# Optimization experiments

Measured on AMD Instinct MI355X. Metric: run time of the kernel, lower is better.

Reference implementation:

```python
import jax, jax.numpy as jnp
import numpy as np

N = 8192          # number of candidate boxes
NUM_CLASSES = 80  # COCO-style class count
IOU_THRESHOLD = 0.45


def setup_inputs() -> dict:
    key = jax.random.key(0)
    k1, k2, k3, k4 = jax.random.split(key, 4)
    # valid xyxy boxes: top-left in [0,1000), width/height in [1,101)
    xy = jax.random.uniform(k1, (N, 2)) * 1000.0
    wh = jax.random.uniform(k2, (N, 2)) * 100.0 + 1.0
    boxes = jnp.concatenate([xy, xy + wh], axis=1)            # [N,4]
    scores = jax.random.uniform(k3, (N,))                     # [N], all > 0
    idxs = jax.random.randint(k4, (N,), 0, NUM_CLASSES)       # [N] class ids
    return {"boxes": boxes, "scores": scores, "idxs": idxs}


def _nms_keep_mask(boxes, scores, iou_thr):
    """Greedy NMS (torchvision semantics) on a single set of boxes.
    Returns a boolean keep mask in the ORIGINAL box order."""
    n = boxes.shape[0]
    order = jnp.argsort(-scores)          # score-descending priority
    b = boxes[order]                      # [n,4]
    area = (b[:, 2] - b[:, 0]) * (b[:, 3] - b[:, 1])
    lt = jnp.maximum(b[:, None, :2], b[None, :, :2])   # [n,n,2]
    rb = jnp.minimum(b[:, None, 2:], b[None, :, 2:])   # [n,n,2]
    wh = jnp.clip(rb - lt, 0.0)
    inter = wh[..., 0] * wh[..., 1]                    # [n,n]
    iou = inter / (area[:, None] + area[None, :] - inter)
    over = iou > iou_thr                               # [n,n] bool
    lower_priority = jnp.arange(n)

    def body(i, suppressed):
        kept_i = jnp.logical_not(suppressed[i])
        # a kept box suppresses all lower-priority boxes it overlaps too much
        return suppressed | (kept_i & over[i] & (lower_priority > i))

    suppressed = jax.lax.fori_loop(0, n, body, jnp.zeros((n,), bool))
    # scatter keep decisions back to original order
    return jnp.zeros((n,), bool).at[order].set(~suppressed)


def reference(boxes, scores, idxs):
    iou_threshold = IOU_THRESHOLD
    # per-class coordinate offsets make boxes of different classes disjoint,
    # so one global NMS == the per-class NMS loop of the torch module
    max_coordinate = boxes.max()
    offsets = idxs.astype(boxes.dtype) * (max_coordinate + 1.0)
    boxes_for_nms = boxes + offsets[:, None]
    keep_mask = _nms_keep_mask(boxes_for_nms, scores, iou_threshold)
    # suppressed boxes get score 0 (all real scores are > 0), so after the
    # descending sort the kept boxes occupy the leading rows exactly as in
    # the torch module; suppressed boxes pad the tail (fixed output shape).
    scores_after_nms = jnp.where(keep_mask, scores, 0.0)
    inds = jnp.argsort(-scores_after_nms)      # [N] keep indices, score-desc
    sorted_scores = scores_after_nms[inds]
    out_boxes = jnp.concatenate([boxes[inds], sorted_scores[:, None]], axis=-1)
    return (out_boxes, inds)
```

## Files before the change

kernel.cpp:

```cpp
#include <hip/hip_runtime.h>
#include <stdint.h>

#define NBOX 8192
#define NW   128
#define IOU_THR 0.45f
#define NCLS 80
#define NSEG NCLS
#define SEGCAP 128
#define CLSCAP 256
#define ENT_LDS 2560
#define TAIL_BLOCKS 8

typedef unsigned long long u64;
typedef unsigned int u32;
typedef unsigned short u16;

__global__ void __launch_bounds__(256) k_pm(const float4* __restrict__ boxes4,
                                            const int* __restrict__ idxs,
                                            const float* __restrict__ scores,
                                            ulonglong2* __restrict__ ent,
                                            u32* __restrict__ entCnt,
                                            u16* __restrict__ rank16g) {
    int b = blockIdx.x, t = threadIdx.x;
    if (b < NCLS) {
        __shared__ float4 lb[CLSCAP];
        __shared__ float  la[CLSCAP];
        __shared__ int    lj[CLSCAP];
        __shared__ float  red[256];
        __shared__ u32    ccnt, lcnt;
        float mx = 0.0f;
        for (int i = t; i < NBOX; i += 256) {
            float4 v = boxes4[i];
            mx = fmaxf(mx, fmaxf(fmaxf(v.x, v.y), fmaxf(v.z, v.w)));
        }
        red[t] = mx;
        __syncthreads();
        for (int s = 128; s > 0; s >>= 1) {
            if (t < s) red[t] = fmaxf(red[t], red[t + s]);
            __syncthreads();
        }
        float mc1 = red[0] + 1.0f;
        float off = (float)b * mc1;
        if (t == 0) { ccnt = 0; lcnt = 0; }
        __syncthreads();
        for (int j = t; j < NBOX; j += 256) {
            if (idxs[j] == b) {
                u32 x = atomicAdd(&ccnt, 1u);
                if (x < CLSCAP) {
                    float4 bx = boxes4[j];
                    bx.x += off; bx.y += off; bx.z += off; bx.w += off;
                    lb[x] = bx;
                    la[x] = (bx.z - bx.x) * (bx.w - bx.y);
                    lj[x] = j;
                }
            }
        }
        __syncthreads();
        u32 cnt = min(ccnt, (u32)CLSCAP);
        if ((u32)t < cnt) {
            float4 bv = lb[t];
            float  av = la[t];
            int    jv = lj[t];
            for (u32 u = 0; u < (u32)t; ++u) {
                float4 bu = lb[u];
                float ltx = fmaxf(bu.x, bv.x), lty = fmaxf(bu.y, bv.y);
                float rbx = fminf(bu.z, bv.z), rby = fminf(bu.w, bv.w);
                float wx = fmaxf(rbx - ltx, 0.0f), wy = fmaxf(rby - lty, 0.0f);
                float inter = wx * wy;
                if (inter > 0.0f) {
                    float iou = inter / (la[u] + av - inter);
                    if (iou > IOU_THR) {
                        u32 x = atomicAdd(&lcnt, 1u);
                        if (x < SEGCAP) {
                            int iu = lj[u];
                            ulonglong2 e;
                            e.x = 1ULL << (iu & 63);
                            e.y = (u64)(((u32)jv << 7) | ((u32)iu >> 6));
                            ent[b * SEGCAP + x] = e;
                        }
                    }
                }
            }
        }
        __syncthreads();
        if (t == 0) entCnt[b] = min(lcnt, (u32)SEGCAP);
    } else {
        __shared__ u64 lk[2048];
        __shared__ u16 part[256];
        int rb = b - NCLS;
        int jj = rb * 32 + (t & 31);
        u64 kj = ((u64)(~__float_as_uint(scores[jj])) << 32) | (u32)jj;
        int cnt = 0;
        int p = t >> 5;
        for (int ch = 0; ch < 4; ++ch) {
            for (int i = t; i < 2048; i += 256) {
                int g = ch * 2048 + i;
                lk[i] = ((u64)(~__float_as_uint(scores[g])) << 32) | (u32)g;
            }
            __syncthreads();
            int base = p * 256;
#pragma unroll 8
            for (int i = 0; i < 256; ++i) cnt += (lk[base + i] < kj) ? 1 : 0;
            __syncthreads();
        }
        part[t] = (u16)cnt;
        __syncthreads();
        if (t < 32) {
            int s = 0;
#pragma unroll
            for (int q = 0; q < 8; ++q) s += part[q * 32 + t];
            rank16g[rb * 32 + t] = (u16)s;
        }
    }
}

__global__ void __launch_bounds__(1024)
k_tail(const ulonglong2* __restrict__ ent, const u32* __restrict__ entCnt,
       const u16* __restrict__ rank16g, const float4* __restrict__ boxes4,
       const float* __restrict__ scores, ulonglong2* __restrict__ gEnt,
       u64* __restrict__ gLT, float* __restrict__ out) {
    __shared__ ulonglong2 sE[ENT_LDS];
    __shared__ u64 sLT[ENT_LDS];
    __shared__ u16 rank16[NBOX];
    __shared__ u32 scnt[NSEG], soff[NSEG];
    __shared__ u64 kw[NW], sup[NW], kws[NW];
    __shared__ u32 wps[NW], wpo[NW];
    __shared__ u32 s_nk;
    __shared__ int chg;

    int t = threadIdx.x;
    if (t < NSEG) scnt[t] = entCnt[t];
    for (int j = t; j < NBOX; j += 1024) rank16[j] = rank16g[j];
    if (t < NW) { kw[t] = ~0ULL; kws[t] = 0ULL; }
    __syncthreads();
    if (t < 64) {
        u32 c0 = (2 * t < NSEG) ? scnt[2 * t] : 0u;
        u32 c1 = (2 * t + 1 < NSEG) ? scnt[2 * t + 1] : 0u;
        u32 s = c0 + c1;
        for (int d = 1; d < 64; d <<= 1) { u32 v = __shfl_up(s, d, 64); if (t >= d) s += v; }
        u32 ex = s - c0 - c1;
        if (2 * t < NSEG) soff[2 * t] = ex;
        if (2 * t + 1 < NSEG) soff[2 * t + 1] = ex + c0;
    }
    __syncthreads();
    u32 n = soff[NSEG - 1] + scnt[NSEG - 1];
    bool fits = (n <= (u32)ENT_LDS);
    for (u32 idx = t; idx < NSEG * SEGCAP; idx += 1024) {
        u32 seg = idx >> 7, l = idx & 127u;
        if (l < scnt[seg]) {
            ulonglong2 E = ent[idx];
            u32 d = soff[seg] + l;
            if (fits) sE[d] = E; else gEnt[d] = E;
        }
    }
    __syncthreads();
    for (u32 e = t; e < n; e += 1024) {
        ulonglong2 E = fits ? sE[e] : gEnt[e];
        u32 meta = (u32)E.y;
        u32 ej = meta >> 7, ew = meta & 127u;
        u32 rj = rank16[ej];
        u64 lt = 0, wrem = E.x;
        while (wrem) {
            int bb = __ffsll(wrem) - 1;
            wrem &= wrem - 1;
            if (rank16[ew * 64 + bb] < rj) lt |= (1ULL << bb);
        }
        if (fits) sLT[e] = lt; else gLT[e] = lt;
    }
    __syncthreads();

    for (int iter = 0; iter < NBOX; ++iter) {
        if (t < NW) sup[t] = 0ULL;
        if (t == 0) chg = 0;
        __syncthreads();
        for (u32 e = t; e < n; e += 1024) {
            ulonglong2 E = fits ? sE[e] : gEnt[e];
            u64 lt      = fits ? sLT[e] : gLT[e];
            u32 meta = (u32)E.y;
            u32 ej = meta >> 7, ew = meta & 127u;
            u64 word = E.x;
            if (word & lt & kw[ew])
                atomicOr(&sup[ej >> 6], 1ULL << (ej & 63u));
            u64 rev = word & ~lt;
            if (rev && ((kw[ej >> 6] >> (ej & 63u)) & 1ULL))
                atomicOr(&sup[ew], rev);
        }
        __syncthreads();
        if (t < NW) {
            u64 nk2 = ~sup[t];
            if (nk2 != kw[t]) { kw[t] = nk2; chg = 1; }
        }
        __syncthreads();
        int dn = !chg;
        __syncthreads();
        if (dn) break;
    }

    for (int j = t; j < NBOX; j += 1024) {
        if ((kw[j >> 6] >> (j & 63)) & 1ULL) {
            u32 r = rank16[j];
            atomicOr(&kws[r >> 6], 1ULL << (r & 63u));
        }
    }
    __syncthreads();
    if (t < 64) {
        int l = t;
        u32 a0 = (u32)__popcll(kws[2 * l]), a1 = (u32)__popcll(kws[2 * l + 1]);
        u32 s = a0 + a1;
        for (int d = 1; d < 64; d <<= 1) { u32 v = __shfl_up(s, d, 64); if (l >= d) s += v; }
        u32 ex = s - a0 - a1;
        wps[2 * l] = ex; wps[2 * l + 1] = ex + a0;
        if (l == 63) s_nk = s;
        u32 b0 = (u32)__popcll(kw[2 * l]), b1 = (u32)__popcll(kw[2 * l + 1]);
        u32 so = b0 + b1;
        for (int d = 1; d < 64; d <<= 1) { u32 v = __shfl_up(so, d, 64); if (l >= d) so += v; }
        u32 exo = so - b0 - b1;
        wpo[2 * l] = exo; wpo[2 * l + 1] = exo + b0;
    }
    __syncthreads();
    u32 nk = s_nk;

    int j = blockIdx.x * 1024 + t;
    if (j < NBOX) {
        bool kept = (kw[j >> 6] >> (j & 63)) & 1ULL;
        u32 pos;
        if (kept) {
            u32 r = rank16[j];
            pos = wps[r >> 6] + (u32)__popcll(kws[r >> 6] & ((1ULL << (r & 63)) - 1ULL));
        } else {
            u32 prefO = wpo[j >> 6] + (u32)__popcll(kw[j >> 6] & ((1ULL << (j & 63)) - 1ULL));
            pos = nk + (u32)j - prefO;
        }
        float4 bx = boxes4[j];
        float s = kept ? scores[j] : 0.0f;
        out[pos * 5 + 0] = bx.x;
        out[pos * 5 + 1] = bx.y;
        out[pos * 5 + 2] = bx.z;
        out[pos * 5 + 3] = bx.w;
        out[pos * 5 + 4] = s;
        out[NBOX * 5 + pos] = (float)j;
    }
}

extern "C" void kernel_launch(void* const* d_in, const int* in_sizes, int n_in,
                              void* d_out, int out_size, void* d_ws, size_t ws_size,
                              hipStream_t stream) {
    const float* boxes  = (const float*)d_in[0];
    const float* scores = (const float*)d_in[1];
    const int*   idxs   = (const int*)d_in[2];
    float* out = (float*)d_out;

    char* w = (char*)d_ws;
    ulonglong2* ent    = (ulonglong2*)(w + 0);
    ulonglong2* gEnt   = (ulonglong2*)(w + 163840);
    u64*        gLT    = (u64*)       (w + 327680);
    u16*        rank16 = (u16*)       (w + 409600);
    u32*        entCnt = (u32*)       (w + 425984);

    k_pm<<<NCLS + 256, 256, 0, stream>>>((const float4*)boxes, idxs, scores, ent, entCnt, rank16);
    k_tail<<<TAIL_BLOCKS, 1024, 0, stream>>>(ent, entCnt, rank16, (const float4*)boxes,
                                             scores, gEnt, gLT, out);
}
```

Baseline: 44.48 us.

## Encode overlap edges as directed winner-loser pairs in a packed u32

Result: slower. 45.73 us (median of 2 runs) (+2.8%).

```diff
diff --git a/kernel.cpp b/kernel.cpp
--- a/kernel.cpp
+++ b/kernel.cpp
@@ -5,10 +5,9 @@
 #define NW   128
 #define IOU_THR 0.45f
 #define NCLS 80
-#define NSEG NCLS
 #define SEGCAP 128
 #define CLSCAP 256
-#define ENT_LDS 2560
+#define EDGE_LDS 2048
 #define TAIL_BLOCKS 8
 
 typedef unsigned long long u64;
@@ -18,13 +17,14 @@
 __global__ void __launch_bounds__(256) k_pm(const float4* __restrict__ boxes4,
                                             const int* __restrict__ idxs,
                                             const float* __restrict__ scores,
-                                            ulonglong2* __restrict__ ent,
+                                            u32* __restrict__ ent,
                                             u32* __restrict__ entCnt,
                                             u16* __restrict__ rank16g) {
     int b = blockIdx.x, t = threadIdx.x;
     if (b < NCLS) {
         __shared__ float4 lb[CLSCAP];
         __shared__ float  la[CLSCAP];
+        __shared__ float  ls[CLSCAP];
         __shared__ int    lj[CLSCAP];
         __shared__ float  red[256];
         __shared__ u32    ccnt, lcnt;
@@ -51,6 +51,7 @@
                     bx.x += off; bx.y += off; bx.z += off; bx.w += off;
                     lb[x] = bx;
                     la[x] = (bx.z - bx.x) * (bx.w - bx.y);
+                    ls[x] = scores[j];
                     lj[x] = j;
                 }
             }
@@ -60,6 +61,7 @@
         if ((u32)t < cnt) {
             float4 bv = lb[t];
             float  av = la[t];
+            float  sv = ls[t];
             int    jv = lj[t];
             for (u32 u = 0; u < (u32)t; ++u) {
                 float4 bu = lb[u];
@@ -70,14 +72,13 @@
                 if (inter > 0.0f) {
                     float iou = inter / (la[u] + av - inter);
                     if (iou > IOU_THR) {
+                        float su = ls[u];
+                        int   iu = lj[u];
+                        bool uwin = (su > sv) || (su == sv && iu < jv);
+                        u32 winI  = uwin ? (u32)iu : (u32)jv;
+                        u32 loseI = uwin ? (u32)jv : (u32)iu;
                         u32 x = atomicAdd(&lcnt, 1u);
-                        if (x < SEGCAP) {
-                            int iu = lj[u];
-                            ulonglong2 e;
-                            e.x = 1ULL << (iu & 63);
-                            e.y = (u64)(((u32)jv << 7) | ((u32)iu >> 6));
-                            ent[b * SEGCAP + x] = e;
-                        }
+                        if (x < SEGCAP) ent[b * SEGCAP + x] = (loseI << 13) | winI;
                     }
                 }
             }
@@ -115,75 +116,42 @@
 }
 
 __global__ void __launch_bounds__(1024)
-k_tail(const ulonglong2* __restrict__ ent, const u32* __restrict__ entCnt,
+k_tail(const u32* __restrict__ ent, const u32* __restrict__ entCnt,
        const u16* __restrict__ rank16g, const float4* __restrict__ boxes4,
-       const float* __restrict__ scores, ulonglong2* __restrict__ gEnt,
-       u64* __restrict__ gLT, float* __restrict__ out) {
-    __shared__ ulonglong2 sE[ENT_LDS];
-    __shared__ u64 sLT[ENT_LDS];
+       const float* __restrict__ scores, float* __restrict__ out) {
+    __shared__ u32 sedge[EDGE_LDS];
     __shared__ u16 rank16[NBOX];
-    __shared__ u32 scnt[NSEG], soff[NSEG];
+    __shared__ u32 scnt[NCLS];
     __shared__ u64 kw[NW], sup[NW], kws[NW];
     __shared__ u32 wps[NW], wpo[NW];
-    __shared__ u32 s_nk;
+    __shared__ u32 s_m, s_nk;
     __shared__ int chg;
 
     int t = threadIdx.x;
-    if (t < NSEG) scnt[t] = entCnt[t];
+    if (t < NCLS) scnt[t] = entCnt[t];
     for (int j = t; j < NBOX; j += 1024) rank16[j] = rank16g[j];
     if (t < NW) { kw[t] = ~0ULL; kws[t] = 0ULL; }
-    __syncthreads();
-    if (t < 64) {
-        u32 c0 = (2 * t < NSEG) ? scnt[2 * t] : 0u;
-        u32 c1 = (2 * t + 1 < NSEG) ? scnt[2 * t + 1] : 0u;
-        u32 s = c0 + c1;
-        for (int d = 1; d < 64; d <<= 1) { u32 v = __shfl_up(s, d, 64); if (t >= d) s += v; }
-        u32 ex = s - c0 - c1;
-        if (2 * t < NSEG) soff[2 * t] = ex;
-        if (2 * t + 1 < NSEG) soff[2 * t + 1] = ex + c0;
-    }
-    __syncthreads();
-    u32 n = soff[NSEG - 1] + scnt[NSEG - 1];
-    bool fits = (n <= (u32)ENT_LDS);
-    for (u32 idx = t; idx < NSEG * SEGCAP; idx += 1024) {
+    if (t == 0) s_m = 0;
+    __syncthreads();
+    for (u32 idx = t; idx < NCLS * SEGCAP; idx += 1024) {
         u32 seg = idx >> 7, l = idx & 127u;
         if (l < scnt[seg]) {
-            ulonglong2 E = ent[idx];
-            u32 d = soff[seg] + l;
-            if (fits) sE[d] = E; else gEnt[d] = E;
-        }
-    }
-    __syncthreads();
-    for (u32 e = t; e < n; e += 1024) {
-        ulonglong2 E = fits ? sE[e] : gEnt[e];
-        u32 meta = (u32)E.y;
-        u32 ej = meta >> 7, ew = meta & 127u;
-        u32 rj = rank16[ej];
-        u64 lt = 0, wrem = E.x;
-        while (wrem) {
-            int bb = __ffsll(wrem) - 1;
-            wrem &= wrem - 1;
-            if (rank16[ew * 64 + bb] < rj) lt |= (1ULL << bb);
-        }
-        if (fits) sLT[e] = lt; else gLT[e] = lt;
-    }
-    __syncthreads();
+            u32 pos = atomicAdd(&s_m, 1u);
+            if (pos < (u32)EDGE_LDS) sedge[pos] = ent[idx];
+        }
+    }
+    __syncthreads();
+    u32 n = min(s_m, (u32)EDGE_LDS);
 
     for (int iter = 0; iter < NBOX; ++iter) {
         if (t < NW) sup[t] = 0ULL;
         if (t == 0) chg = 0;
         __syncthreads();
         for (u32 e = t; e < n; e += 1024) {
-            ulonglong2 E = fits ? sE[e] : gEnt[e];
-            u64 lt      = fits ? sLT[e] : gLT[e];
-            u32 meta = (u32)E.y;
-            u32 ej = meta >> 7, ew = meta & 127u;
-            u64 word = E.x;
-            if (word & lt & kw[ew])
-                atomicOr(&sup[ej >> 6], 1ULL << (ej & 63u));
-            u64 rev = word & ~lt;
-            if (rev && ((kw[ej >> 6] >> (ej & 63u)) & 1ULL))
-                atomicOr(&sup[ew], rev);
+            u32 ed = sedge[e];
+            u32 winI = ed & 8191u, loseI = ed >> 13;
+            if ((kw[winI >> 6] >> (winI & 63u)) & 1ULL)
+                atomicOr(&sup[loseI >> 6], 1ULL << (loseI & 63u));
         }
         __syncthreads();
         if (t < NW) {
@@ -251,13 +219,11 @@
     float* out = (float*)d_out;
 
     char* w = (char*)d_ws;
-    ulonglong2* ent    = (ulonglong2*)(w + 0);
-    ulonglong2* gEnt   = (ulonglong2*)(w + 163840);
-    u64*        gLT    = (u64*)       (w + 327680);
-    u16*        rank16 = (u16*)       (w + 409600);
-    u32*        entCnt = (u32*)       (w + 425984);
+    u32* ent    = (u32*)(w + 0);
+    u16* rank16 = (u16*)(w + 40960);
+    u32* entCnt = (u32*)(w + 57344);
 
     k_pm<<<NCLS + 256, 256, 0, stream>>>((const float4*)boxes, idxs, scores, ent, entCnt, rank16);
     k_tail<<<TAIL_BLOCKS, 1024, 0, stream>>>(ent, entCnt, rank16, (const float4*)boxes,
-                                             scores, gEnt, gLT, out);
+                                             scores, out);
 }
```
